# Kernel optimization log

Hardware: AMD Instinct MI355X
Metric: run time of the kernel (lower is better)

Reference implementation:

```python
import jax, jax.numpy as jnp
import numpy as np

N_LAYERS = 32
HIDDEN = 1024
INTER = 2816
BATCH = 256
INIT_SCALE = 0.02


def setup_inputs() -> dict:
    key = jax.random.key(0)
    k_h, k_g, k_u, k_d = jax.random.split(key, 4)
    down_std = INIT_SCALE / np.sqrt(2 * N_LAYERS)
    h = jax.random.normal(k_h, (BATCH, N_LAYERS, HIDDEN), dtype=jnp.float32)
    # torch Linear weight layout: (out_features, in_features); stack over experts
    Wg = jax.random.normal(k_g, (N_LAYERS, INTER, HIDDEN), dtype=jnp.float32) * INIT_SCALE
    Wu = jax.random.normal(k_u, (N_LAYERS, INTER, HIDDEN), dtype=jnp.float32) * INIT_SCALE
    Wd = jax.random.normal(k_d, (N_LAYERS, HIDDEN, INTER), dtype=jnp.float32) * down_std
    return {"h": h, "Wg": Wg, "Wu": Wu, "Wd": Wd}


def reference(h, Wg, Wu, Wd):
    # h: (B, N, D); Wg/Wu: (N, I, D); Wd: (N, D, I)
    gate = jnp.einsum("bnd,nid->bni", h, Wg)
    up = jnp.einsum("bnd,nid->bni", h, Wu)
    act = jax.nn.silu(gate) * up            # (B, N, I)
    out = jnp.einsum("bni,ndi->bnd", act, Wd)  # (B, N, D)
    return out
```

## Files before the change

kernel.cpp:

```cpp
#include <hip/hip_runtime.h>
#include <hip/hip_bf16.h>

#define BATCH   256
#define NLAYERS 32
#define HID     1024
#define INTER   2816
#define BK      64

typedef __attribute__((ext_vector_type(8))) short bf16x8;
typedef __attribute__((ext_vector_type(4))) float f32x4;
typedef __attribute__((ext_vector_type(4))) int   i32x4;

__device__ __forceinline__ ushort f2bf(float f) {
  __hip_bfloat16 b = __float2bfloat16(f);
  return *reinterpret_cast<ushort*>(&b);
}

__device__ __forceinline__ bf16x8 cvt8(f32x4 a, f32x4 b) {
  bf16x8 o;
  o[0] = (short)f2bf(a[0]); o[1] = (short)f2bf(a[1]);
  o[2] = (short)f2bf(a[2]); o[3] = (short)f2bf(a[3]);
  o[4] = (short)f2bf(b[0]); o[5] = (short)f2bf(b[1]);
  o[6] = (short)f2bf(b[2]); o[7] = (short)f2bf(b[3]);
  return o;
}

__global__ __launch_bounds__(256) void k_pack(
    const float* __restrict__ h, ushort* __restrict__ Xp) {
  const int r    = blockIdx.x * 4 + (threadIdx.x >> 6);
  const int lane = threadIdx.x & 63;
  const int ro   = ((r & 31) * 256 + (r >> 5)) * 1024;
  const float* src = h + (size_t)r * 1024 + lane * 4;
  ushort* dst      = Xp + ro + lane * 4;
#pragma unroll
  for (int g = 0; g < 4; ++g) {
    f32x4 v = *(const f32x4*)(src + g * 256);
    ushort4 o;
    o.x = f2bf(v[0]); o.y = f2bf(v[1]); o.z = f2bf(v[2]); o.w = f2bf(v[3]);
    *(ushort4*)(dst + g * 256) = o;
  }
}

__global__ __launch_bounds__(512, 4) void k_gateup(
    const ushort* __restrict__ Xp, const float* __restrict__ Wg,
    const float* __restrict__ Wu, ushort* __restrict__ act) {
  const int bid   = blockIdx.x;
  const int layer = bid / (INTER / 64);
  const int it    = bid % (INTER / 64);
  const int i0    = it * 64;
  const int tid   = threadIdx.x;
  const int lane  = tid & 63;
  const int wave  = tid >> 6;
  const int wm    = wave >> 1;
  const int wn    = wave & 1;

  __shared__ ushort lds[BATCH * BK + 128 * BK];
  ushort* Al = lds;
  ushort* Wl = lds + BATCH * BK;

  f32x4 acc[4][2][2] = {};

  int aldst[4];
  const ushort* asrc[4];
#pragma unroll
  for (int r = 0; r < 4; ++r) {
    int g = tid + 512 * r;
    int arow = g >> 3, akc = g & 7;
    aldst[r] = arow * BK + ((akc ^ (arow & 7)) << 3);
    asrc[r] = Xp + ((size_t)layer * BATCH + arow) * HID + akc * 8;
  }
  const int wrow = tid >> 3, wsl = tid & 7;
  const int wldstG = wrow * BK + ((wsl ^ (wrow & 7)) << 3);
  const int wrowU  = 64 + wrow;
  const int wldstU = wrowU * BK + ((wsl ^ (wrowU & 7)) << 3);
  const float* gsrc = Wg + (size_t)layer * INTER * HID + (size_t)(i0 + wrow) * HID + wsl * 8;
  const float* usrc = Wu + (size_t)layer * INTER * HID + (size_t)(i0 + wrow) * HID + wsl * 8;

  i32x4 ra[4];
  f32x4 rg[2], ru[2];
#pragma unroll
  for (int r = 0; r < 4; ++r) ra[r] = *(const i32x4*)asrc[r];
  rg[0] = *(const f32x4*)gsrc; rg[1] = *(const f32x4*)(gsrc + 4);
  ru[0] = *(const f32x4*)usrc; ru[1] = *(const f32x4*)(usrc + 4);

  const int r16 = lane & 15;
  const int g4  = lane >> 4;

  const int NK = HID / BK;
  for (int k = 0; k < NK; ++k) {
    __syncthreads();
#pragma unroll
    for (int r = 0; r < 4; ++r) *(i32x4*)&Al[aldst[r]] = ra[r];
    *(bf16x8*)&Wl[wldstG] = cvt8(rg[0], rg[1]);
    *(bf16x8*)&Wl[wldstU] = cvt8(ru[0], ru[1]);
    __syncthreads();

    if (k + 1 < NK) {
      int off = (k + 1) * BK;
#pragma unroll
      for (int r = 0; r < 4; ++r) ra[r] = *(const i32x4*)(asrc[r] + off);
      rg[0] = *(const f32x4*)(gsrc + off); rg[1] = *(const f32x4*)(gsrc + off + 4);
      ru[0] = *(const f32x4*)(usrc + off); ru[1] = *(const f32x4*)(usrc + off + 4);
    }

#pragma unroll
    for (int ks = 0; ks < 2; ++ks) {
      const int kg = ks * 4 + g4;
      bf16x8 af[4];
#pragma unroll
      for (int m = 0; m < 4; ++m) {
        int row = wm * 64 + m * 16 + r16;
        af[m] = *(bf16x8*)&Al[row * BK + ((kg ^ (row & 7)) << 3)];
      }
#pragma unroll
      for (int n = 0; n < 2; ++n) {
        int rowG = wn * 32 + n * 16 + r16;
        int rowU = 64 + rowG;
        bf16x8 bg = *(bf16x8*)&Wl[rowG * BK + ((kg ^ (rowG & 7)) << 3)];
        bf16x8 bu = *(bf16x8*)&Wl[rowU * BK + ((kg ^ (rowU & 7)) << 3)];
#pragma unroll
        for (int m = 0; m < 4; ++m) {
          acc[m][n][0] = __builtin_amdgcn_mfma_f32_16x16x32_bf16(af[m], bg, acc[m][n][0], 0, 0, 0);
          acc[m][n][1] = __builtin_amdgcn_mfma_f32_16x16x32_bf16(af[m], bu, acc[m][n][1], 0, 0, 0);
        }
      }
    }
  }

  const int r4 = (lane >> 4) * 4;
#pragma unroll
  for (int m = 0; m < 4; ++m)
#pragma unroll
    for (int n = 0; n < 2; ++n)
#pragma unroll
      for (int r = 0; r < 4; ++r) {
        float g = acc[m][n][0][r];
        float u = acc[m][n][1][r];
        float a = (g / (1.f + __expf(-g))) * u;
        int b = wm * 64 + m * 16 + r4 + r;
        int i = i0 + wn * 32 + n * 16 + r16;
        act[((size_t)layer * BATCH + b) * INTER + i] = f2bf(a);
      }
}

__global__ __launch_bounds__(512) void k_down(
    const ushort* __restrict__ act, const float* __restrict__ Wd,
    float* __restrict__ out) {
  const int bid   = blockIdx.x;
  const int layer = bid / (HID / 64);
  const int dtile = bid % (HID / 64);
  const int d0    = dtile * 64;
  const int tid   = threadIdx.x;
  const int lane  = tid & 63;
  const int wave  = tid >> 6;
  const int wm    = wave >> 1;
  const int wn    = wave & 1;

  __shared__ ushort lds[BATCH * BK + 64 * BK];
  ushort* Al = lds;
  ushort* Wl = lds + BATCH * BK;

  f32x4 acc[4][2] = {};

  int aldst[4];
  const ushort* asrc[4];
#pragma unroll
  for (int r = 0; r < 4; ++r) {
    int g = tid + 512 * r;
    int arow = g >> 3, akc = g & 7;
    aldst[r] = arow * BK + ((akc ^ (arow & 7)) << 3);
    asrc[r] = act + ((size_t)layer * BATCH + arow) * INTER + akc * 8;
  }
  const int wrow = tid >> 3, wkc = tid & 7;
  const int wldst = wrow * BK + ((wkc ^ (wrow & 7)) << 3);
  const float* wsrc = Wd + (size_t)layer * HID * INTER + (size_t)(d0 + wrow) * INTER + wkc * 8;

  i32x4 ra[4];
  f32x4 rw[2];

#pragma unroll
  for (int r = 0; r < 4; ++r) ra[r] = *(const i32x4*)asrc[r];
  rw[0] = *(const f32x4*)wsrc; rw[1] = *(const f32x4*)(wsrc + 4);

  const int NK = INTER / BK;
  for (int k = 0; k < NK; ++k) {
    __syncthreads();
#pragma unroll
    for (int r = 0; r < 4; ++r) *(i32x4*)&Al[aldst[r]] = ra[r];
    *(bf16x8*)&Wl[wldst] = cvt8(rw[0], rw[1]);
    __syncthreads();

    if (k + 1 < NK) {
      int off = (k + 1) * BK;
#pragma unroll
      for (int r = 0; r < 4; ++r) ra[r] = *(const i32x4*)(asrc[r] + off);
      rw[0] = *(const f32x4*)(wsrc + off); rw[1] = *(const f32x4*)(wsrc + off + 4);
    }

#pragma unroll
    for (int ks = 0; ks < 2; ++ks) {
      const int kg = ks * 4 + (lane >> 4);
      bf16x8 af[4];
#pragma unroll
      for (int m = 0; m < 4; ++m) {
        int row = wm * 64 + m * 16 + (lane & 15);
        af[m] = *(bf16x8*)&Al[row * BK + ((kg ^ (row & 7)) << 3)];
      }
#pragma unroll
      for (int n = 0; n < 2; ++n) {
        int row = wn * 32 + n * 16 + (lane & 15);
        bf16x8 bw = *(bf16x8*)&Wl[row * BK + ((kg ^ (row & 7)) << 3)];
#pragma unroll
        for (int m = 0; m < 4; ++m)
          acc[m][n] = __builtin_amdgcn_mfma_f32_16x16x32_bf16(af[m], bw, acc[m][n], 0, 0, 0);
      }
    }
  }

  const int c16 = lane & 15;
  const int r4  = (lane >> 4) * 4;
#pragma unroll
  for (int m = 0; m < 4; ++m)
#pragma unroll
    for (int n = 0; n < 2; ++n)
#pragma unroll
      for (int r = 0; r < 4; ++r) {
        int b = wm * 64 + m * 16 + r4 + r;
        int d = d0 + wn * 32 + n * 16 + c16;
        out[(size_t)b * (NLAYERS * HID) + (size_t)layer * HID + d] = acc[m][n][r];
      }
}

extern "C" void kernel_launch(void* const* d_in, const int* in_sizes, int n_in,
                              void* d_out, int out_size, void* d_ws, size_t ws_size,
                              hipStream_t stream) {
  const float* h  = (const float*)d_in[0];
  const float* Wg = (const float*)d_in[1];
  const float* Wu = (const float*)d_in[2];
  const float* Wd = (const float*)d_in[3];
  float* out  = (float*)d_out;
  ushort* act = (ushort*)d_ws;
  ushort* Xp  = (ushort*)d_ws + (size_t)NLAYERS * BATCH * INTER;

  hipLaunchKernelGGL(k_pack, dim3(BATCH * NLAYERS / 4), dim3(256), 0, stream,
                     h, Xp);
  hipLaunchKernelGGL(k_gateup, dim3(NLAYERS * (INTER / 64)), dim3(512), 0, stream,
                     Xp, Wg, Wu, act);
  hipLaunchKernelGGL(k_down, dim3(NLAYERS * (HID / 64)), dim3(512), 0, stream,
                     act, Wd, out);
}
```

Before: 337.5 us.

## Double-buffer gate/up GEMM with direct global-to-LDS loads and pre-swizzled activations

```diff
diff --git a/kernel.cpp b/kernel.cpp
--- a/kernel.cpp
+++ b/kernel.cpp
@@ -5,7 +5,6 @@
 #define NLAYERS 32
 #define HID     1024
 #define INTER   2816
-#define BK      64
 
 typedef __attribute__((ext_vector_type(8))) short bf16x8;
 typedef __attribute__((ext_vector_type(4))) float f32x4;
@@ -26,23 +25,26 @@
 }
 
 __global__ __launch_bounds__(256) void k_pack(
-    const float* __restrict__ h, ushort* __restrict__ Xp) {
-  const int r    = blockIdx.x * 4 + (threadIdx.x >> 6);
-  const int lane = threadIdx.x & 63;
-  const int ro   = ((r & 31) * 256 + (r >> 5)) * 1024;
-  const float* src = h + (size_t)r * 1024 + lane * 4;
-  ushort* dst      = Xp + ro + lane * 4;
-#pragma unroll
-  for (int g = 0; g < 4; ++g) {
-    f32x4 v = *(const f32x4*)(src + g * 256);
-    ushort4 o;
-    o.x = f2bf(v[0]); o.y = f2bf(v[1]); o.z = f2bf(v[2]); o.w = f2bf(v[3]);
-    *(ushort4*)(dst + g * 256) = o;
+    const float* __restrict__ h, ushort* __restrict__ Xp2) {
+  const int pr    = blockIdx.x * 4 + (threadIdx.x >> 6);
+  const int b     = pr >> 5;
+  const int layer = pr & 31;
+  const int lane  = threadIdx.x & 63;
+  const float* src = h + (size_t)b * (NLAYERS * HID) + (size_t)layer * HID;
+  ushort* dstL = Xp2 + (size_t)layer * (32 * 8192);
+#pragma unroll
+  for (int c = 0; c < 2; ++c) {
+    int gi = lane + c * 64;
+    int t  = gi >> 2, kg = gi & 3;
+    f32x4 v0 = *(const f32x4*)(src + t * 32 + kg * 8);
+    f32x4 v1 = *(const f32x4*)(src + t * 32 + kg * 8 + 4);
+    int f = kg ^ ((b >> 1) & 3);
+    *(bf16x8*)(dstL + (size_t)t * 8192 + b * 32 + f * 8) = cvt8(v0, v1);
   }
 }
 
 __global__ __launch_bounds__(512, 4) void k_gateup(
-    const ushort* __restrict__ Xp, const float* __restrict__ Wg,
+    const ushort* __restrict__ Xp2, const float* __restrict__ Wg,
     const float* __restrict__ Wu, ushort* __restrict__ act) {
   const int bid   = blockIdx.x;
   const int layer = bid / (INTER / 64);
@@ -53,78 +55,74 @@
   const int wave  = tid >> 6;
   const int wm    = wave >> 1;
   const int wn    = wave & 1;
-
-  __shared__ ushort lds[BATCH * BK + 128 * BK];
-  ushort* Al = lds;
-  ushort* Wl = lds + BATCH * BK;
+  const int r16   = lane & 15;
+  const int g4    = lane >> 4;
+
+  __shared__ ushort Al[2][256 * 32];
+  __shared__ ushort Bl[2][128 * 32];
 
   f32x4 acc[4][2][2] = {};
 
-  int aldst[4];
-  const ushort* asrc[4];
-#pragma unroll
-  for (int r = 0; r < 4; ++r) {
-    int g = tid + 512 * r;
-    int arow = g >> 3, akc = g & 7;
-    aldst[r] = arow * BK + ((akc ^ (arow & 7)) << 3);
-    asrc[r] = Xp + ((size_t)layer * BATCH + arow) * HID + akc * 8;
-  }
-  const int wrow = tid >> 3, wsl = tid & 7;
-  const int wldstG = wrow * BK + ((wsl ^ (wrow & 7)) << 3);
-  const int wrowU  = 64 + wrow;
-  const int wldstU = wrowU * BK + ((wsl ^ (wrowU & 7)) << 3);
-  const float* gsrc = Wg + (size_t)layer * INTER * HID + (size_t)(i0 + wrow) * HID + wsl * 8;
-  const float* usrc = Wu + (size_t)layer * INTER * HID + (size_t)(i0 + wrow) * HID + wsl * 8;
-
-  i32x4 ra[4];
-  f32x4 rg[2], ru[2];
-#pragma unroll
-  for (int r = 0; r < 4; ++r) ra[r] = *(const i32x4*)asrc[r];
-  rg[0] = *(const f32x4*)gsrc; rg[1] = *(const f32x4*)(gsrc + 4);
-  ru[0] = *(const f32x4*)usrc; ru[1] = *(const f32x4*)(usrc + 4);
-
-  const int r16 = lane & 15;
-  const int g4  = lane >> 4;
-
-  const int NK = HID / BK;
-  for (int k = 0; k < NK; ++k) {
+  const int brow  = tid >> 2;
+  const int bslot = tid & 3;
+  const int bdst  = brow * 32 + ((bslot ^ ((brow >> 1) & 3)) << 3);
+  const float* bsrc = (brow < 64 ? Wg + (size_t)(i0 + brow) * HID
+                                 : Wu + (size_t)(i0 + brow - 64) * HID)
+                      + (size_t)layer * INTER * HID + bslot * 8;
+
+  const ushort* agbase = Xp2 + (size_t)layer * (32 * 8192);
+
+#pragma unroll
+  for (int c = 0; c < 2; ++c)
+    __builtin_amdgcn_global_load_lds(
+        (const void*)(agbase + (wave * 128 + c * 64 + lane) * 8),
+        (void*)&Al[0][(wave * 128 + c * 64) * 8], 16, 0, 0);
+  {
+    f32x4 rb0 = *(const f32x4*)bsrc;
+    f32x4 rb1 = *(const f32x4*)(bsrc + 4);
+    *(bf16x8*)&Bl[0][bdst] = cvt8(rb0, rb1);
+  }
+  __syncthreads();
+
+  const int NK = HID / 32;
+  int cur = 0;
+  for (int t = 0; t < NK; ++t) {
+    const int nxt = cur ^ 1;
+    f32x4 rb[2];
+    if (t + 1 < NK) {
+#pragma unroll
+      for (int c = 0; c < 2; ++c)
+        __builtin_amdgcn_global_load_lds(
+            (const void*)(agbase + (size_t)(t + 1) * 8192 +
+                          (wave * 128 + c * 64 + lane) * 8),
+            (void*)&Al[nxt][(wave * 128 + c * 64) * 8], 16, 0, 0);
+      rb[0] = *(const f32x4*)(bsrc + (t + 1) * 32);
+      rb[1] = *(const f32x4*)(bsrc + (t + 1) * 32 + 4);
+    }
+
+    bf16x8 af[4];
+#pragma unroll
+    for (int m = 0; m < 4; ++m) {
+      int row = wm * 64 + m * 16 + r16;
+      af[m] = *(bf16x8*)&Al[cur][row * 32 + ((g4 ^ ((row >> 1) & 3)) << 3)];
+    }
+#pragma unroll
+    for (int n = 0; n < 2; ++n) {
+      int rg_ = wn * 32 + n * 16 + r16;
+      int ru_ = 64 + rg_;
+      bf16x8 bg = *(bf16x8*)&Bl[cur][rg_ * 32 + ((g4 ^ ((rg_ >> 1) & 3)) << 3)];
+      bf16x8 bu = *(bf16x8*)&Bl[cur][ru_ * 32 + ((g4 ^ ((ru_ >> 1) & 3)) << 3)];
+#pragma unroll
+      for (int m = 0; m < 4; ++m) {
+        acc[m][n][0] = __builtin_amdgcn_mfma_f32_16x16x32_bf16(af[m], bg, acc[m][n][0], 0, 0, 0);
+        acc[m][n][1] = __builtin_amdgcn_mfma_f32_16x16x32_bf16(af[m], bu, acc[m][n][1], 0, 0, 0);
+      }
+    }
+
+    if (t + 1 < NK)
+      *(bf16x8*)&Bl[nxt][bdst] = cvt8(rb[0], rb[1]);
     __syncthreads();
-#pragma unroll
-    for (int r = 0; r < 4; ++r) *(i32x4*)&Al[aldst[r]] = ra[r];
-    *(bf16x8*)&Wl[wldstG] = cvt8(rg[0], rg[1]);
-    *(bf16x8*)&Wl[wldstU] = cvt8(ru[0], ru[1]);
-    __syncthreads();
-
-    if (k + 1 < NK) {
-      int off = (k + 1) * BK;
-#pragma unroll
-      for (int r = 0; r < 4; ++r) ra[r] = *(const i32x4*)(asrc[r] + off);
-      rg[0] = *(const f32x4*)(gsrc + off); rg[1] = *(const f32x4*)(gsrc + off + 4);
-      ru[0] = *(const f32x4*)(usrc + off); ru[1] = *(const f32x4*)(usrc + off + 4);
-    }
-
-#pragma unroll
-    for (int ks = 0; ks < 2; ++ks) {
-      const int kg = ks * 4 + g4;
-      bf16x8 af[4];
-#pragma unroll
-      for (int m = 0; m < 4; ++m) {
-        int row = wm * 64 + m * 16 + r16;
-        af[m] = *(bf16x8*)&Al[row * BK + ((kg ^ (row & 7)) << 3)];
-      }
-#pragma unroll
-      for (int n = 0; n < 2; ++n) {
-        int rowG = wn * 32 + n * 16 + r16;
-        int rowU = 64 + rowG;
-        bf16x8 bg = *(bf16x8*)&Wl[rowG * BK + ((kg ^ (rowG & 7)) << 3)];
-        bf16x8 bu = *(bf16x8*)&Wl[rowU * BK + ((kg ^ (rowU & 7)) << 3)];
-#pragma unroll
-        for (int m = 0; m < 4; ++m) {
-          acc[m][n][0] = __builtin_amdgcn_mfma_f32_16x16x32_bf16(af[m], bg, acc[m][n][0], 0, 0, 0);
-          acc[m][n][1] = __builtin_amdgcn_mfma_f32_16x16x32_bf16(af[m], bu, acc[m][n][1], 0, 0, 0);
-        }
-      }
-    }
+    cur = nxt;
   }
 
   const int r4 = (lane >> 4) * 4;
@@ -142,6 +140,8 @@
         act[((size_t)layer * BATCH + b) * INTER + i] = f2bf(a);
       }
 }
+
+#define BK 64
 
 __global__ __launch_bounds__(512) void k_down(
     const ushort* __restrict__ act, const float* __restrict__ Wd,
@@ -240,12 +240,12 @@
   const float* Wd = (const float*)d_in[3];
   float* out  = (float*)d_out;
   ushort* act = (ushort*)d_ws;
-  ushort* Xp  = (ushort*)d_ws + (size_t)NLAYERS * BATCH * INTER;
+  ushort* Xp2 = (ushort*)d_ws + (size_t)NLAYERS * BATCH * INTER;
 
   hipLaunchKernelGGL(k_pack, dim3(BATCH * NLAYERS / 4), dim3(256), 0, stream,
-                     h, Xp);
+                     h, Xp2);
   hipLaunchKernelGGL(k_gateup, dim3(NLAYERS * (INTER / 64)), dim3(512), 0, stream,
-                     Xp, Wg, Wu, act);
+                     Xp2, Wg, Wu, act);
   hipLaunchKernelGGL(k_down, dim3(NLAYERS * (HID / 64)), dim3(512), 0, stream,
                      act, Wd, out);
 }
```

After: 324.8 us. -3.7%, faster.
